# Kernel optimization log

Hardware: AMD Instinct MI355X
Metric: run time of the kernel (lower is better)

## Reference

```python
import jax, jax.numpy as jnp
from jax import lax
import numpy as np

VOCAB, EMB, U1, U2 = 50000, 200, 400, 200
B, T = 128, 256
BN_EPS = 1e-3  # Keras BatchNormalization default epsilon


def _gru(x, mask, W, U, b, units):
    """Keras GRU, reset_after=True, zero_output_for_mask=False.
    x: [B,T,D], mask: [B,T] bool, W: [D,3u], U: [u,3u], b: [2,3u]."""
    bi, br = b[0], b[1]
    xw = jnp.einsum('btd,dk->btk', x, W) + bi          # precompute input projections [B,T,3u]
    xs = jnp.swapaxes(xw, 0, 1)                        # [T,B,3u]
    ms = jnp.swapaxes(mask, 0, 1)                      # [T,B]

    def step(h, inp):
        xt, mt = inp
        rec = h @ U + br                               # [B,3u]
        xz, xr, xh = jnp.split(xt, 3, axis=-1)
        rz, rr, rh = jnp.split(rec, 3, axis=-1)
        z = jax.nn.sigmoid(xz + rz)                    # update gate
        r = jax.nn.sigmoid(xr + rr)                    # reset gate
        hh = jnp.tanh(xh + r * rh)                     # candidate (reset_after)
        h_new = z * h + (1.0 - z) * hh
        h = jnp.where(mt[:, None], h_new, h)           # masked steps carry state/output
        return h, h

    h0 = jnp.zeros((x.shape[0], units), x.dtype)
    hT, outs = lax.scan(step, h0, (xs, ms))
    return jnp.swapaxes(outs, 0, 1), hT


def setup_inputs() -> dict:
    key = jax.random.key(0)
    ks = jax.random.split(key, 12)
    f32 = jnp.float32
    return {
        'tokens': jax.random.randint(ks[0], (B, T), 0, VOCAB),
        'emb': jax.random.normal(ks[1], (VOCAB, EMB), f32) * 0.02,
        'gamma': jnp.ones((EMB,), f32),
        'beta': jnp.zeros((EMB,), f32),
        'mmean': jax.random.normal(ks[2], (EMB,), f32) * 0.01,
        'mvar': jax.random.uniform(ks[3], (EMB,), f32, 0.5, 1.5),
        'W1': jax.random.normal(ks[4], (EMB, 3 * U1), f32) * 0.02,
        'Ur1': jax.random.normal(ks[5], (U1, 3 * U1), f32) * 0.02,
        'b1': jnp.zeros((2, 3 * U1), f32),
        'W2': jax.random.normal(ks[6], (U1, 3 * U2), f32) * 0.02,
        'Ur2': jax.random.normal(ks[7], (U2, 3 * U2), f32) * 0.02,
        'b2': jnp.zeros((2, 3 * U2), f32),
    }


def reference(tokens, emb, gamma, beta, mmean, mvar, W1, Ur1, b1, W2, Ur2, b2):
    mask = tokens != 0                                  # mask_zero=True
    x = emb[tokens]                                     # [B,T,200]
    # BatchNorm (inference: moving stats)
    x = (x - mmean) * lax.rsqrt(mvar + BN_EPS) * gamma + beta
    out1, h1 = _gru(x, mask, W1, Ur1, b1, U1)           # [B,T,400], [B,400]
    out2, h2 = _gru(out1, mask, W2, Ur2, b2, U2)        # [B,T,200], [B,200]
    return (out2, out1, h2, h1)
```

## Files before the change

kernel.cpp:

```cpp
#include <hip/hip_runtime.h>

typedef unsigned int u32;
typedef unsigned short u16;
typedef unsigned long long u64;

typedef __attribute__((ext_vector_type(8))) short bf16x8;
typedef __attribute__((ext_vector_type(4))) float f32x4;

__device__ __forceinline__ u16 f2bf(float f) {
    u32 u = __float_as_uint(f);
    u += 0x7fffu + ((u >> 16) & 1u);
    return (u16)(u >> 16);
}
__device__ __forceinline__ float bf2f(u16 h) {
    return __uint_as_float(((u32)h) << 16);
}

__global__ __launch_bounds__(256) void prep_kernel(
    const float* __restrict__ W1, const float* __restrict__ W2,
    const float* __restrict__ U1, const float* __restrict__ U2,
    u16* __restrict__ W1T, u16* __restrict__ W2T,
    u16* __restrict__ U1T, u16* __restrict__ U2T,
    u32* __restrict__ hzero)
{
    int i = blockIdx.x * 256 + threadIdx.x;
    if (i < 240000) { int j = i / 200, k = i - j * 200; W1T[i] = f2bf(W1[k * 1200 + j]); return; }
    i -= 240000;
    if (i < 240000) { int j = i / 400, k = i - j * 400; W2T[i] = f2bf(W2[k * 600 + j]); return; }
    i -= 240000;
    if (i < 480000) { int j = i / 400, k = i - j * 400; U1T[i] = f2bf(U1[k * 1200 + j]); return; }
    i -= 480000;
    if (i < 120000) { int j = i / 200, k = i - j * 200; U2T[i] = f2bf(U2[k * 600 + j]); return; }
    i -= 120000;
    if (i < 307232) hzero[i] = 0u;
}

__global__ __launch_bounds__(256) void embed_bn_kernel(
    const int* __restrict__ tokens, const float* __restrict__ emb,
    const float* __restrict__ gamma, const float* __restrict__ beta,
    const float* __restrict__ mmean, const float* __restrict__ mvar,
    u16* __restrict__ x)
{
    int gid = blockIdx.x * 256 + threadIdx.x;
    int r = gid / 200, e = gid - r * 200;
    int t = r >> 7, b = r & 127;
    int tok = tokens[b * 256 + t];
    float v = (emb[(size_t)tok * 200 + e] - mmean[e]) *
              (1.0f / sqrtf(mvar[e] + 1e-3f)) * gamma[e] + beta[e];
    x[gid] = f2bf(v);
}

template<int KEL, int KSTEPS, int KPAD>
__global__ __launch_bounds__(256) void gemm_bias_kernel(
    const u16* __restrict__ A, const u16* __restrict__ BT,
    const float* __restrict__ bias, u16* __restrict__ C, int N)
{
    __shared__ u16 A_lds[64 * KPAD];
    __shared__ u16 B_lds[64 * KPAD];
    const int m0 = blockIdx.x * 64, n0 = blockIdx.y * 64;
    const int tid = threadIdx.x;
    const int lane = tid & 63, wave = tid >> 6;
    const int l15 = lane & 15, lq = lane >> 4;

    for (int idx = tid; idx < 64 * (KPAD / 2); idx += 256) {
        int row = idx / (KPAD / 2), kp = idx % (KPAD / 2);
        int k = kp * 2;
        u32 va = (k < KEL) ? *(const u32*)(A + (size_t)(m0 + row) * KEL + k) : 0u;
        *(u32*)(A_lds + row * KPAD + k) = va;
        int gn = n0 + row;
        u32 vb = (k < KEL && gn < N) ? *(const u32*)(BT + (size_t)gn * KEL + k) : 0u;
        *(u32*)(B_lds + row * KPAD + k) = vb;
    }
    __syncthreads();

    f32x4 acc[4];
    for (int i = 0; i < 4; ++i) acc[i] = (f32x4){0.f, 0.f, 0.f, 0.f};
    for (int ks = 0; ks < KSTEPS; ++ks) {
        bf16x8 a = *(const bf16x8*)(A_lds + (wave * 16 + l15) * KPAD + ks * 32 + lq * 8);
        for (int nt = 0; nt < 4; ++nt) {
            bf16x8 b = *(const bf16x8*)(B_lds + (nt * 16 + l15) * KPAD + ks * 32 + lq * 8);
            acc[nt] = __builtin_amdgcn_mfma_f32_16x16x32_bf16(a, b, acc[nt], 0, 0, 0);
        }
    }
    for (int nt = 0; nt < 4; ++nt) {
        int col = n0 + nt * 16 + l15;
        if (col < N) {
            float bv = bias[col];
            for (int i = 0; i < 4; ++i) {
                int row = m0 + wave * 16 + lq * 4 + i;
                C[(size_t)row * N + col] = f2bf(acc[nt][i] + bv);
            }
        }
    }
}

__global__ __launch_bounds__(256) void fused_gru_kernel(
    const u16* __restrict__ xw1,
    const u16* __restrict__ U1T,
    const float* __restrict__ br1,
    const u16* __restrict__ W2T,
    const u16* __restrict__ U2T,
    const float* __restrict__ b2,
    const int* __restrict__ tokens,
    float* __restrict__ out1,
    u16* __restrict__ o1b,
    float* __restrict__ h1f,
    float* __restrict__ out2,
    float* __restrict__ h2f,
    u32* __restrict__ hbuf1,
    u32* __restrict__ hbuf2,
    u32* __restrict__ ctrl)
{
    __shared__ __align__(16) char smem[140288];
    __shared__ int claim_s[3];
    const int tid = threadIdx.x;

    if (tid == 0) {
        u32 xcc;
        asm volatile("s_getreg_b32 %0, hwreg(HW_REG_XCC_ID)" : "=s"(xcc));
        int x = (int)(xcc & 7u);
        int role = -1, cg = -1, cw = -1;
        for (int a = 0; a < 8 && role < 0; ++a) {
            int gg = (x + a) & 7;
            u32 ww = atomicAdd(&ctrl[gg], 1u);
            if (ww < 16u) { role = 0; cg = gg; cw = (int)ww; }
        }
        for (int a = 0; a < 8 && role < 0; ++a) {
            int gg = (x + a) & 7;
            u32 ww = atomicAdd(&ctrl[8 + gg], 1u);
            if (ww < 8u) { role = 1; cg = gg; cw = (int)ww; }
        }
        claim_s[0] = role; claim_s[1] = cg; claim_s[2] = cw;
    }
    __syncthreads();
    const int role = claim_s[0], g = claim_s[1], w = claim_s[2];
    const int b0 = g * 16;
    const int lane = tid & 63, wave = tid >> 6;
    const int l15 = lane & 15, lq = lane >> 4;

    if (role == 0) {
        u16* U_lds = (u16*)smem;
        u16* h_lds = (u16*)(smem + 67840);
        float* rec_lds = (float*)(smem + 81408);
        unsigned char* tok_lds = (unsigned char*)(smem + 86528);

        for (int i = tid; i < 16960; i += 256) ((u32*)U_lds)[i] = 0u;
        for (int i = tid; i < 3392; i += 256) ((u32*)h_lds)[i] = 0u;
        __syncthreads();
        for (int idx = tid; idx < 15000; idx += 256) {
            int c = idx / 200, kp = idx - (idx / 200) * 200;
            int j = (c / 25) * 400 + w * 25 + (c % 25);
            *(u32*)(U_lds + c * 424 + kp * 2) =
                *(const u32*)(U1T + (size_t)j * 400 + kp * 2);
        }
        for (int i = tid; i < 4096; i += 256) {
            int b = i >> 8, tt = i & 255;
            tok_lds[i] = (tokens[(b0 + b) * 256 + tt] != 0) ? 1 : 0;
        }

        int ne = 0;
        int eb[2], eco[2], eih[2], egb[2], exw[2];
        float ebrz[2], ebrr[2], ebrh[2], hold[2];
        for (int u = tid; u < 400; u += 256) {
            int b = u / 25, co = u % 25;
            int ih = w * 25 + co;
            eb[ne] = b; eco[ne] = co; eih[ne] = ih; egb[ne] = b0 + b;
            exw[ne] = (b0 + b) * 1200;
            ebrz[ne] = br1[ih]; ebrr[ne] = br1[400 + ih]; ebrh[ne] = br1[800 + ih];
            hold[ne] = 0.f; ++ne;
        }
        u32 pend0 = 0; int soff[13], loff[13];
        for (int i = 0; i < 13; ++i) {
            int s = tid + i * 256;
            if (s < 3200) {
                int b = s / 200, kk = s % 200;
                soff[i] = b * 400 + kk * 2; loff[i] = b * 424 + kk * 2;
                pend0 |= 1u << i;
            } else { soff[i] = 0; loff[i] = 0; }
        }
        u32* hb = hbuf1 + (size_t)g * 4 * 16 * 400;

        for (int t = 0; t < 256; ++t) {
            float xzv[2], xrv[2], xhv[2];
            for (int e = 0; e < ne; ++e) {
                const u16* xr = xw1 + (size_t)t * 153600 + exw[e];
                xzv[e] = bf2f(xr[eih[e]]);
                xrv[e] = bf2f(xr[400 + eih[e]]);
                xhv[e] = bf2f(xr[800 + eih[e]]);
            }
            const u32* hsrc = hb + (t & 3) * 6400;
            const u32 want = (u32)t & 0xFFFFu;
            u32 pend = pend0;
            while (pend) {
                u64 tmp[13];
                #pragma unroll
                for (int i = 0; i < 13; ++i)
                    if (pend & (1u << i))
                        tmp[i] = __hip_atomic_load((const u64*)(hsrc + soff[i]),
                                                   __ATOMIC_RELAXED,
                                                   __HIP_MEMORY_SCOPE_AGENT);
                #pragma unroll
                for (int i = 0; i < 13; ++i)
                    if (pend & (1u << i)) {
                        u64 v = tmp[i];
                        if ((u32)(v & 0xFFFFu) == want &&
                            ((u32)(v >> 32) & 0xFFFFu) == want) {
                            *(u32*)(h_lds + loff[i]) =
                                ((u32)(v >> 16) & 0xFFFFu) | ((u32)(v >> 48) << 16);
                            pend &= ~(1u << i);
                        }
                    }
                if (pend) __builtin_amdgcn_s_sleep(1);
            }
            __syncthreads();

            f32x4 acc[2];
            acc[0] = (f32x4){0.f, 0.f, 0.f, 0.f};
            acc[1] = (f32x4){0.f, 0.f, 0.f, 0.f};
            for (int ks = 0; ks < 13; ++ks) {
                bf16x8 a = *(const bf16x8*)(h_lds + l15 * 424 + ks * 32 + lq * 8);
                int ti = 0;
                for (int nt = wave; nt < 5; nt += 4, ++ti) {
                    bf16x8 b = *(const bf16x8*)(U_lds + (nt * 16 + l15) * 424 + ks * 32 + lq * 8);
                    acc[ti] = __builtin_amdgcn_mfma_f32_16x16x32_bf16(a, b, acc[ti], 0, 0, 0);
                }
            }
            {
                int ti = 0;
                for (int nt = wave; nt < 5; nt += 4, ++ti)
                    for (int i = 0; i < 4; ++i)
                        rec_lds[(lq * 4 + i) * 80 + nt * 16 + l15] = acc[ti][i];
            }
            __syncthreads();

            u32* hdst = hb + ((t + 1) & 3) * 6400;
            float hnv[2]; u32 tgv[2];
            for (int e = 0; e < ne; ++e) {
                int b = eb[e], co = eco[e];
                float rz = rec_lds[b * 80 + co] + ebrz[e];
                float rr = rec_lds[b * 80 + 25 + co] + ebrr[e];
                float rh = rec_lds[b * 80 + 50 + co] + ebrh[e];
                float z = 1.f / (1.f + __expf(-(xzv[e] + rz)));
                float r = 1.f / (1.f + __expf(-(xrv[e] + rr)));
                float pre = xhv[e] + r * rh;
                float th = 2.f / (1.f + __expf(-2.f * pre)) - 1.f;
                float hn = z * hold[e] + (1.f - z) * th;
                if (!tok_lds[b * 256 + t]) hn = hold[e];
                hold[e] = hn; hnv[e] = hn;
                tgv[e] = ((u32)f2bf(hn) << 16) | (u32)(t + 1);
            }
            for (int e = 0; e < ne; ++e)
                __hip_atomic_store(hdst + eb[e] * 400 + eih[e], tgv[e],
                                   __ATOMIC_RELAXED, __HIP_MEMORY_SCOPE_AGENT);
            for (int e = 0; e < ne; ++e) {
                int gb = egb[e], ih = eih[e];
                out1[((size_t)gb * 256 + t) * 400 + ih] = hnv[e];
                o1b[(size_t)(t * 128 + gb) * 400 + ih] = (u16)(tgv[e] >> 16);
                if (t == 255) h1f[(size_t)gb * 400 + ih] = hnv[e];
            }
            asm volatile("s_waitcnt vmcnt(0)" ::: "memory");
            __syncthreads();
            if (tid == 0)
                __hip_atomic_fetch_add(&ctrl[16 + g], 1u, __ATOMIC_RELAXED,
                                       __HIP_MEMORY_SCOPE_AGENT);
        }
    } else {
        u16* W2_lds = (u16*)smem;
        u16* U2_lds = (u16*)(smem + 67840);
        u16* o1_lds = (u16*)(smem + 104960);
        u16* h2_lds = (u16*)(smem + 118528);
        float* xw_lds = (float*)(smem + 125952);
        float* rc_lds = (float*)(smem + 131072);
        unsigned char* tok_lds = (unsigned char*)(smem + 136192);

        for (int i = tid; i < 31488; i += 256) ((u32*)smem)[i] = 0u;
        __syncthreads();
        for (int idx = tid; idx < 15000; idx += 256) {
            int c = idx / 200, kp = idx - (idx / 200) * 200;
            int j = (c / 25) * 200 + w * 25 + (c % 25);
            *(u32*)(W2_lds + c * 424 + kp * 2) =
                *(const u32*)(W2T + (size_t)j * 400 + kp * 2);
        }
        for (int idx = tid; idx < 7500; idx += 256) {
            int c = idx / 100, kp = idx - (idx / 100) * 100;
            int j = (c / 25) * 200 + w * 25 + (c % 25);
            *(u32*)(U2_lds + c * 232 + kp * 2) =
                *(const u32*)(U2T + (size_t)j * 200 + kp * 2);
        }
        for (int i = tid; i < 4096; i += 256) {
            int b = i >> 8, tt = i & 255;
            tok_lds[i] = (tokens[(b0 + b) * 256 + tt] != 0) ? 1 : 0;
        }

        int ne = 0;
        int eb[2], eco[2], eih[2], egb[2];
        float ebiz[2], ebir[2], ebih[2], ebrz[2], ebrr[2], ebrh[2], hold[2];
        for (int u = tid; u < 400; u += 256) {
            int b = u / 25, co = u % 25;
            int ih = w * 25 + co;
            eb[ne] = b; eco[ne] = co; eih[ne] = ih; egb[ne] = b0 + b;
            ebiz[ne] = b2[ih];       ebir[ne] = b2[200 + ih];  ebih[ne] = b2[400 + ih];
            ebrz[ne] = b2[600 + ih]; ebrr[ne] = b2[800 + ih];  ebrh[ne] = b2[1000 + ih];
            hold[ne] = 0.f; ++ne;
        }
        u32 pend0 = 0; int soff[7], loff[7];
        for (int i = 0; i < 7; ++i) {
            int s = tid + i * 256;
            if (s < 1600) {
                int b = s / 100, kk = s % 100;
                soff[i] = b * 200 + kk * 2; loff[i] = b * 232 + kk * 2;
                pend0 |= 1u << i;
            } else { soff[i] = 0; loff[i] = 0; }
        }
        u32* hb = hbuf2 + (size_t)g * 4 * 16 * 200;
        __syncthreads();

        for (int t = 0; t < 256; ++t) {
            const u32 need = 16u * (u32)(t + 1);
            while (__hip_atomic_load(&ctrl[16 + g], __ATOMIC_RELAXED,
                                     __HIP_MEMORY_SCOPE_AGENT) < need)
                __builtin_amdgcn_s_sleep(2);
            asm volatile("" ::: "memory");

            const u32* src = (const u32*)(o1b + (size_t)(t * 128 + b0) * 400);
            for (int idx = tid; idx < 3200; idx += 256) {
                int row = idx / 200, k = idx - row * 200;
                *(u32*)(o1_lds + row * 424 + k * 2) = src[idx];
            }

            const u32* hsrc = hb + (t & 3) * 3200;
            const u32 want = (u32)t & 0xFFFFu;
            u32 pend = pend0;
            while (pend) {
                u64 tmp[7];
                #pragma unroll
                for (int i = 0; i < 7; ++i)
                    if (pend & (1u << i))
                        tmp[i] = __hip_atomic_load((const u64*)(hsrc + soff[i]),
                                                   __ATOMIC_RELAXED,
                                                   __HIP_MEMORY_SCOPE_AGENT);
                #pragma unroll
                for (int i = 0; i < 7; ++i)
                    if (pend & (1u << i)) {
                        u64 v = tmp[i];
                        if ((u32)(v & 0xFFFFu) == want &&
                            ((u32)(v >> 32) & 0xFFFFu) == want) {
                            *(u32*)(h2_lds + loff[i]) =
                                ((u32)(v >> 16) & 0xFFFFu) | ((u32)(v >> 48) << 16);
                            pend &= ~(1u << i);
                        }
                    }
                if (pend) __builtin_amdgcn_s_sleep(1);
            }
            __syncthreads();

            f32x4 aw[2], au[2];
            aw[0] = (f32x4){0.f,0.f,0.f,0.f}; aw[1] = (f32x4){0.f,0.f,0.f,0.f};
            au[0] = (f32x4){0.f,0.f,0.f,0.f}; au[1] = (f32x4){0.f,0.f,0.f,0.f};
            for (int ks = 0; ks < 13; ++ks) {
                bf16x8 a = *(const bf16x8*)(o1_lds + l15 * 424 + ks * 32 + lq * 8);
                int ti = 0;
                for (int nt = wave; nt < 5; nt += 4, ++ti) {
                    bf16x8 b = *(const bf16x8*)(W2_lds + (nt * 16 + l15) * 424 + ks * 32 + lq * 8);
                    aw[ti] = __builtin_amdgcn_mfma_f32_16x16x32_bf16(a, b, aw[ti], 0, 0, 0);
                }
            }
            for (int ks = 0; ks < 7; ++ks) {
                bf16x8 a = *(const bf16x8*)(h2_lds + l15 * 232 + ks * 32 + lq * 8);
                int ti = 0;
                for (int nt = wave; nt < 5; nt += 4, ++ti) {
                    bf16x8 b = *(const bf16x8*)(U2_lds + (nt * 16 + l15) * 232 + ks * 32 + lq * 8);
                    au[ti] = __builtin_amdgcn_mfma_f32_16x16x32_bf16(a, b, au[ti], 0, 0, 0);
                }
            }
            {
                int ti = 0;
                for (int nt = wave; nt < 5; nt += 4, ++ti)
                    for (int i = 0; i < 4; ++i) {
                        xw_lds[(lq * 4 + i) * 80 + nt * 16 + l15] = aw[ti][i];
                        rc_lds[(lq * 4 + i) * 80 + nt * 16 + l15] = au[ti][i];
                    }
            }
            __syncthreads();

            u32* hdst = hb + ((t + 1) & 3) * 3200;
            float hnv[2]; u32 tgv[2];
            for (int e = 0; e < ne; ++e) {
                int b = eb[e], co = eco[e];
                float xz = xw_lds[b * 80 + co] + ebiz[e];
                float rz = rc_lds[b * 80 + co] + ebrz[e];
                float xr = xw_lds[b * 80 + 25 + co] + ebir[e];
                float rr = rc_lds[b * 80 + 25 + co] + ebrr[e];
                float xh = xw_lds[b * 80 + 50 + co] + ebih[e];
                float rh = rc_lds[b * 80 + 50 + co] + ebrh[e];
                float z = 1.f / (1.f + __expf(-(xz + rz)));
                float r = 1.f / (1.f + __expf(-(xr + rr)));
                float pre = xh + r * rh;
                float th = 2.f / (1.f + __expf(-2.f * pre)) - 1.f;
                float hn = z * hold[e] + (1.f - z) * th;
                if (!tok_lds[b * 256 + t]) hn = hold[e];
                hold[e] = hn; hnv[e] = hn;
                tgv[e] = ((u32)f2bf(hn) << 16) | (u32)(t + 1);
            }
            for (int e = 0; e < ne; ++e)
                __hip_atomic_store(hdst + eb[e] * 200 + eih[e], tgv[e],
                                   __ATOMIC_RELAXED, __HIP_MEMORY_SCOPE_AGENT);
            for (int e = 0; e < ne; ++e) {
                int gb = egb[e], ih = eih[e];
                out2[((size_t)gb * 256 + t) * 200 + ih] = hnv[e];
                if (t == 255) h2f[(size_t)gb * 200 + ih] = hnv[e];
            }
        }
    }
}

extern "C" void kernel_launch(void* const* d_in, const int* in_sizes, int n_in,
                              void* d_out, int out_size, void* d_ws, size_t ws_size,
                              hipStream_t stream)
{
    const int*   tokens = (const int*)d_in[0];
    const float* emb    = (const float*)d_in[1];
    const float* gamma  = (const float*)d_in[2];
    const float* beta   = (const float*)d_in[3];
    const float* mmean  = (const float*)d_in[4];
    const float* mvar   = (const float*)d_in[5];
    const float* W1     = (const float*)d_in[6];
    const float* U1     = (const float*)d_in[7];
    const float* b1     = (const float*)d_in[8];
    const float* W2     = (const float*)d_in[9];
    const float* U2     = (const float*)d_in[10];
    const float* b2     = (const float*)d_in[11];

    float* out = (float*)d_out;
    char* ws = (char*)d_ws;

    u16* x     = (u16*)(ws + 0);
    u16* xw1   = (u16*)(ws + 13107200);
    u16* o1b   = (u16*)(ws + 91750400);
    u16* W1T   = (u16*)(ws + 157286400);
    u16* W2T   = (u16*)(ws + 157766400);
    u16* U1T   = (u16*)(ws + 158246400);
    u16* U2T   = (u16*)(ws + 159206400);
    u32* hbuf1 = (u32*)(ws + 159446400);
    u32* hbuf2 = (u32*)(ws + 160265600);
    u32* ctrl  = (u32*)(ws + 160675200);

    float* out2 = out;
    float* out1 = out + 6553600;
    float* h2   = out + 19660800;
    float* h1   = out + 19686400;

    prep_kernel<<<5420, 256, 0, stream>>>(W1, W2, U1, U2, W1T, W2T, U1T, U2T,
                                          hbuf1);
    embed_bn_kernel<<<25600, 256, 0, stream>>>(tokens, emb, gamma, beta, mmean,
                                               mvar, x);
    gemm_bias_kernel<200, 7, 232><<<dim3(512, 19), 256, 0, stream>>>(
        x, W1T, b1, xw1, 1200);
    fused_gru_kernel<<<192, 256, 0, stream>>>(
        xw1, U1T, b1 + 1200, W2T, U2T, b2, tokens,
        out1, o1b, h1, out2, h2, hbuf1, hbuf2, ctrl);
}
```

Before: 2.209 ms.

## Replace per-element tag polling with counter-based barriers and full-history h buffer

Layer-1 blocks now wait on a per-group arrival counter and then do plain loads of the hidden state, instead of repeatedly polling every tagged element. The layer-1 hidden history is kept in a 256-slot ring, and layer 2 reads its input directly from it, which removes the separate o1b bf16 copy and its stores. Layer 2 likewise gets its own counter for its recurrent state, with an 8-deep ring. The intent is to cut polling traffic and the redundant output copy on the sequential critical path. In exchange, each step adds a counter fetch-add plus a barrier, and the hbuf1 workspace becomes much larger.

```diff
diff --git a/kernel.cpp b/kernel.cpp
--- a/kernel.cpp
+++ b/kernel.cpp
@@ -21,7 +21,7 @@
     const float* __restrict__ U1, const float* __restrict__ U2,
     u16* __restrict__ W1T, u16* __restrict__ W2T,
     u16* __restrict__ U1T, u16* __restrict__ U2T,
-    u32* __restrict__ hzero)
+    u32* __restrict__ hb1, u32* __restrict__ hb2, u32* __restrict__ ctrl)
 {
     int i = blockIdx.x * 256 + threadIdx.x;
     if (i < 240000) { int j = i / 200, k = i - j * 200; W1T[i] = f2bf(W1[k * 1200 + j]); return; }
@@ -32,7 +32,19 @@
     i -= 480000;
     if (i < 120000) { int j = i / 200, k = i - j * 200; U2T[i] = f2bf(U2[k * 600 + j]); return; }
     i -= 120000;
-    if (i < 307232) hzero[i] = 0u;
+    if (i < 51200) {
+        int gg = i / 6400;
+        hb1[(size_t)gg * 1638400 + (i - gg * 6400)] = 0u;
+        return;
+    }
+    i -= 51200;
+    if (i < 25600) {
+        int gg = i / 3200;
+        hb2[gg * 25600 + (i - gg * 3200)] = 0u;
+        return;
+    }
+    i -= 25600;
+    if (i < 32) ctrl[i] = 0u;
 }
 
 __global__ __launch_bounds__(256) void embed_bn_kernel(
@@ -103,7 +115,6 @@
     const float* __restrict__ b2,
     const int* __restrict__ tokens,
     float* __restrict__ out1,
-    u16* __restrict__ o1b,
     float* __restrict__ h1f,
     float* __restrict__ out2,
     float* __restrict__ h2f,
@@ -169,16 +180,12 @@
             ebrz[ne] = br1[ih]; ebrr[ne] = br1[400 + ih]; ebrh[ne] = br1[800 + ih];
             hold[ne] = 0.f; ++ne;
         }
-        u32 pend0 = 0; int soff[13], loff[13];
+        int loff[13];
         for (int i = 0; i < 13; ++i) {
             int s = tid + i * 256;
-            if (s < 3200) {
-                int b = s / 200, kk = s % 200;
-                soff[i] = b * 400 + kk * 2; loff[i] = b * 424 + kk * 2;
-                pend0 |= 1u << i;
-            } else { soff[i] = 0; loff[i] = 0; }
-        }
-        u32* hb = hbuf1 + (size_t)g * 4 * 16 * 400;
+            loff[i] = (s < 3200) ? ((s / 200) * 424 + (s % 200) * 2) : 0;
+        }
+        u32* hb = hbuf1 + (size_t)g * 1638400;
 
         for (int t = 0; t < 256; ++t) {
             float xzv[2], xrv[2], xhv[2];
@@ -188,29 +195,22 @@
                 xrv[e] = bf2f(xr[400 + eih[e]]);
                 xhv[e] = bf2f(xr[800 + eih[e]]);
             }
-            const u32* hsrc = hb + (t & 3) * 6400;
-            const u32 want = (u32)t & 0xFFFFu;
-            u32 pend = pend0;
-            while (pend) {
-                u64 tmp[13];
-                #pragma unroll
-                for (int i = 0; i < 13; ++i)
-                    if (pend & (1u << i))
-                        tmp[i] = __hip_atomic_load((const u64*)(hsrc + soff[i]),
-                                                   __ATOMIC_RELAXED,
-                                                   __HIP_MEMORY_SCOPE_AGENT);
-                #pragma unroll
-                for (int i = 0; i < 13; ++i)
-                    if (pend & (1u << i)) {
-                        u64 v = tmp[i];
-                        if ((u32)(v & 0xFFFFu) == want &&
-                            ((u32)(v >> 32) & 0xFFFFu) == want) {
-                            *(u32*)(h_lds + loff[i]) =
-                                ((u32)(v >> 16) & 0xFFFFu) | ((u32)(v >> 48) << 16);
-                            pend &= ~(1u << i);
-                        }
-                    }
-                if (pend) __builtin_amdgcn_s_sleep(1);
+
+            const u32 need = 16u * (u32)t;
+            while (__hip_atomic_load(&ctrl[16 + g], __ATOMIC_RELAXED,
+                                     __HIP_MEMORY_SCOPE_AGENT) < need)
+                __builtin_amdgcn_s_sleep(1);
+            asm volatile("" ::: "memory");
+
+            const u64* src = (const u64*)(hb + (size_t)t * 6400);
+            #pragma unroll
+            for (int i = 0; i < 13; ++i) {
+                int s = tid + i * 256;
+                if (s < 3200) {
+                    u64 v = src[s];
+                    *(u32*)(h_lds + loff[i]) =
+                        ((u32)(v >> 16) & 0xFFFFu) | ((u32)(v >> 48) << 16);
+                }
             }
             __syncthreads();
 
@@ -233,7 +233,7 @@
             }
             __syncthreads();
 
-            u32* hdst = hb + ((t + 1) & 3) * 6400;
+            u32* hd = hb + (size_t)((t + 1) & 255) * 6400;
             float hnv[2]; u32 tgv[2];
             for (int e = 0; e < ne; ++e) {
                 int b = eb[e], co = eco[e];
@@ -250,19 +250,18 @@
                 tgv[e] = ((u32)f2bf(hn) << 16) | (u32)(t + 1);
             }
             for (int e = 0; e < ne; ++e)
-                __hip_atomic_store(hdst + eb[e] * 400 + eih[e], tgv[e],
+                __hip_atomic_store(hd + eb[e] * 400 + eih[e], tgv[e],
                                    __ATOMIC_RELAXED, __HIP_MEMORY_SCOPE_AGENT);
+            asm volatile("s_waitcnt vmcnt(0)" ::: "memory");
+            __syncthreads();
+            if (tid == 0)
+                __hip_atomic_fetch_add(&ctrl[16 + g], 1u, __ATOMIC_RELAXED,
+                                       __HIP_MEMORY_SCOPE_AGENT);
             for (int e = 0; e < ne; ++e) {
                 int gb = egb[e], ih = eih[e];
                 out1[((size_t)gb * 256 + t) * 400 + ih] = hnv[e];
-                o1b[(size_t)(t * 128 + gb) * 400 + ih] = (u16)(tgv[e] >> 16);
                 if (t == 255) h1f[(size_t)gb * 400 + ih] = hnv[e];
             }
-            asm volatile("s_waitcnt vmcnt(0)" ::: "memory");
-            __syncthreads();
-            if (tid == 0)
-                __hip_atomic_fetch_add(&ctrl[16 + g], 1u, __ATOMIC_RELAXED,
-                                       __HIP_MEMORY_SCOPE_AGENT);
         }
     } else {
         u16* W2_lds = (u16*)smem;
@@ -303,54 +302,52 @@
             ebrz[ne] = b2[600 + ih]; ebrr[ne] = b2[800 + ih];  ebrh[ne] = b2[1000 + ih];
             hold[ne] = 0.f; ++ne;
         }
-        u32 pend0 = 0; int soff[7], loff[7];
+        int loffA[13], loffB[7];
+        for (int i = 0; i < 13; ++i) {
+            int s = tid + i * 256;
+            loffA[i] = (s < 3200) ? ((s / 200) * 424 + (s % 200) * 2) : 0;
+        }
         for (int i = 0; i < 7; ++i) {
             int s = tid + i * 256;
-            if (s < 1600) {
-                int b = s / 100, kk = s % 100;
-                soff[i] = b * 200 + kk * 2; loff[i] = b * 232 + kk * 2;
-                pend0 |= 1u << i;
-            } else { soff[i] = 0; loff[i] = 0; }
-        }
-        u32* hb = hbuf2 + (size_t)g * 4 * 16 * 200;
+            loffB[i] = (s < 1600) ? ((s / 100) * 232 + (s % 100) * 2) : 0;
+        }
+        u32* hb1g = hbuf1 + (size_t)g * 1638400;
+        u32* hb2 = hbuf2 + g * 25600;
         __syncthreads();
 
         for (int t = 0; t < 256; ++t) {
-            const u32 need = 16u * (u32)(t + 1);
+            const u32 need1 = 16u * (u32)(t + 1);
             while (__hip_atomic_load(&ctrl[16 + g], __ATOMIC_RELAXED,
-                                     __HIP_MEMORY_SCOPE_AGENT) < need)
+                                     __HIP_MEMORY_SCOPE_AGENT) < need1)
                 __builtin_amdgcn_s_sleep(2);
             asm volatile("" ::: "memory");
 
-            const u32* src = (const u32*)(o1b + (size_t)(t * 128 + b0) * 400);
-            for (int idx = tid; idx < 3200; idx += 256) {
-                int row = idx / 200, k = idx - row * 200;
-                *(u32*)(o1_lds + row * 424 + k * 2) = src[idx];
-            }
-
-            const u32* hsrc = hb + (t & 3) * 3200;
-            const u32 want = (u32)t & 0xFFFFu;
-            u32 pend = pend0;
-            while (pend) {
-                u64 tmp[7];
-                #pragma unroll
-                for (int i = 0; i < 7; ++i)
-                    if (pend & (1u << i))
-                        tmp[i] = __hip_atomic_load((const u64*)(hsrc + soff[i]),
-                                                   __ATOMIC_RELAXED,
-                                                   __HIP_MEMORY_SCOPE_AGENT);
-                #pragma unroll
-                for (int i = 0; i < 7; ++i)
-                    if (pend & (1u << i)) {
-                        u64 v = tmp[i];
-                        if ((u32)(v & 0xFFFFu) == want &&
-                            ((u32)(v >> 32) & 0xFFFFu) == want) {
-                            *(u32*)(h2_lds + loff[i]) =
-                                ((u32)(v >> 16) & 0xFFFFu) | ((u32)(v >> 48) << 16);
-                            pend &= ~(1u << i);
-                        }
-                    }
-                if (pend) __builtin_amdgcn_s_sleep(1);
+            const u64* srcA = (const u64*)(hb1g + (size_t)((t + 1) & 255) * 6400);
+            #pragma unroll
+            for (int i = 0; i < 13; ++i) {
+                int s = tid + i * 256;
+                if (s < 3200) {
+                    u64 v = srcA[s];
+                    *(u32*)(o1_lds + loffA[i]) =
+                        ((u32)(v >> 16) & 0xFFFFu) | ((u32)(v >> 48) << 16);
+                }
+            }
+
+            const u32 need2 = 8u * (u32)t;
+            while (__hip_atomic_load(&ctrl[24 + g], __ATOMIC_RELAXED,
+                                     __HIP_MEMORY_SCOPE_AGENT) < need2)
+                __builtin_amdgcn_s_sleep(1);
+            asm volatile("" ::: "memory");
+            const u64* srcB = (const u64*)(hb2 + (size_t)(t & 7) * 3200);
+            #pragma unroll
+            for (int i = 0; i < 7; ++i) {
+                int s = tid + i * 256;
+                if (s < 1600) {
+                    u64 v = __hip_atomic_load(srcB + s, __ATOMIC_RELAXED,
+                                              __HIP_MEMORY_SCOPE_AGENT);
+                    *(u32*)(h2_lds + loffB[i]) =
+                        ((u32)(v >> 16) & 0xFFFFu) | ((u32)(v >> 48) << 16);
+                }
             }
             __syncthreads();
 
@@ -383,7 +380,7 @@
             }
             __syncthreads();
 
-            u32* hdst = hb + ((t + 1) & 3) * 3200;
+            u32* hd = hb2 + (size_t)((t + 1) & 7) * 3200;
             float hnv[2]; u32 tgv[2];
             for (int e = 0; e < ne; ++e) {
                 int b = eb[e], co = eco[e];
@@ -403,8 +400,13 @@
                 tgv[e] = ((u32)f2bf(hn) << 16) | (u32)(t + 1);
             }
             for (int e = 0; e < ne; ++e)
-                __hip_atomic_store(hdst + eb[e] * 200 + eih[e], tgv[e],
+                __hip_atomic_store(hd + eb[e] * 200 + eih[e], tgv[e],
                                    __ATOMIC_RELAXED, __HIP_MEMORY_SCOPE_AGENT);
+            asm volatile("s_waitcnt vmcnt(0)" ::: "memory");
+            __syncthreads();
+            if (tid == 0)
+                __hip_atomic_fetch_add(&ctrl[24 + g], 1u, __ATOMIC_RELAXED,
+                                       __HIP_MEMORY_SCOPE_AGENT);
             for (int e = 0; e < ne; ++e) {
                 int gb = egb[e], ih = eih[e];
                 out2[((size_t)gb * 256 + t) * 200 + ih] = hnv[e];
@@ -436,27 +438,26 @@
 
     u16* x     = (u16*)(ws + 0);
     u16* xw1   = (u16*)(ws + 13107200);
-    u16* o1b   = (u16*)(ws + 91750400);
-    u16* W1T   = (u16*)(ws + 157286400);
-    u16* W2T   = (u16*)(ws + 157766400);
-    u16* U1T   = (u16*)(ws + 158246400);
-    u16* U2T   = (u16*)(ws + 159206400);
-    u32* hbuf1 = (u32*)(ws + 159446400);
-    u32* hbuf2 = (u32*)(ws + 160265600);
-    u32* ctrl  = (u32*)(ws + 160675200);
+    u16* W1T   = (u16*)(ws + 91750400);
+    u16* W2T   = (u16*)(ws + 92230400);
+    u16* U1T   = (u16*)(ws + 92710400);
+    u16* U2T   = (u16*)(ws + 93670400);
+    u32* hbuf1 = (u32*)(ws + 93910400);
+    u32* hbuf2 = (u32*)(ws + 146339200);
+    u32* ctrl  = (u32*)(ws + 147158400);
 
     float* out2 = out;
     float* out1 = out + 6553600;
     float* h2   = out + 19660800;
     float* h1   = out + 19686400;
 
-    prep_kernel<<<5420, 256, 0, stream>>>(W1, W2, U1, U2, W1T, W2T, U1T, U2T,
-                                          hbuf1);
+    prep_kernel<<<4519, 256, 0, stream>>>(W1, W2, U1, U2, W1T, W2T, U1T, U2T,
+                                          hbuf1, hbuf2, ctrl);
     embed_bn_kernel<<<25600, 256, 0, stream>>>(tokens, emb, gamma, beta, mmean,
                                                mvar, x);
     gemm_bias_kernel<200, 7, 232><<<dim3(512, 19), 256, 0, stream>>>(
         x, W1T, b1, xw1, 1200);
     fused_gru_kernel<<<192, 256, 0, stream>>>(
         xw1, U1T, b1 + 1200, W2T, U2T, b2, tokens,
-        out1, o1b, h1, out2, h2, hbuf1, hbuf2, ctrl);
-}
+        out1, h1, out2, h2, hbuf1, hbuf2, ctrl);
+}
```

Result: slower. 2.394 ms (+8.4%).
